# Performance work log

Hardware: AMD Instinct MI355X
Metric: run time of the kernel (lower is better)

## Reference

```python
import jax, jax.numpy as jnp
import numpy as np

B, S, D = 4, 2048, 1024
H = 8  # hardcoded in AttentionLayer
HD = D // H
FF = 4096
EPS = 1e-5


def _layernorm(x):
    # LayerNorm(hidden_dim, elementwise_affine=False), eps=1e-5
    mu = jnp.mean(x, axis=-1, keepdims=True)
    var = jnp.var(x, axis=-1, keepdims=True)
    return (x - mu) / jnp.sqrt(var + EPS)


def setup_inputs() -> dict:
    key = jax.random.key(0)
    ks = jax.random.split(key, 5)
    scale = 0.02
    return {
        "x": jax.random.normal(ks[0], (B, S, D), dtype=jnp.float32),
        "qkv_proj": jax.random.normal(ks[1], (D, 3 * D), dtype=jnp.float32) * scale,
        "o_proj": jax.random.normal(ks[2], (D, D), dtype=jnp.float32) * scale,
        "ff1": jax.random.normal(ks[3], (D, FF), dtype=jnp.float32) * scale,
        "ff2": jax.random.normal(ks[4], (FF, D), dtype=jnp.float32) * scale,
    }


def reference(x, qkv_proj, o_proj, ff1, ff2):
    b, s, d = x.shape
    # --- attention ---
    qkv = jnp.matmul(x, qkv_proj)                       # [b,s,3d]
    qkv = qkv.reshape(b, s, H, 3 * HD).transpose(0, 2, 1, 3)  # [b,h,s,3hd]
    q, k, v = jnp.split(qkv, 3, axis=-1)                # each [b,h,s,hd]
    logits = jnp.einsum('bhqd,bhkd->bhqk', q, k) / jnp.sqrt(jnp.float32(HD))
    attn = jax.nn.softmax(logits, axis=-1)
    vals = jnp.einsum('bhqk,bhkd->bhqd', attn, v)       # [b,h,s,hd]
    vals = vals.transpose(0, 2, 1, 3).reshape(b, s, d)
    attn_out = jnp.matmul(vals, o_proj)
    # --- residual + norm + FFN + residual + norm ---
    x = _layernorm(x + attn_out)
    ff_out = jnp.matmul(jax.nn.relu(jnp.matmul(x, ff1)), ff2)
    x = _layernorm(x + ff_out)
    return x
```

## Files before the change

kernel.cpp:

```cpp
#include <hip/hip_runtime.h>
#include <hip/hip_bf16.h>


typedef float floatx4 __attribute__((ext_vector_type(4)));
typedef float floatx16 __attribute__((ext_vector_type(16)));
typedef short bf16x8 __attribute__((ext_vector_type(8)));

#define DEVI __device__ __forceinline__

typedef const __attribute__((address_space(1))) unsigned int* gas1_t;
typedef __attribute__((address_space(3))) unsigned int* las3_t;

DEVI void gll16(const void* g, void* l) {
  __builtin_amdgcn_global_load_lds((gas1_t)g, (las3_t)l, 16, 0, 0);
}

DEVI short bfbits(float f) {
  __hip_bfloat16 h = __float2bfloat16(f);
  return *reinterpret_cast<short*>(&h);
}

DEVI unsigned int packbf(float lo, float hi) {
  return __builtin_amdgcn_perm(__float_as_uint(hi) + 0x8000u,
                               __float_as_uint(lo) + 0x8000u,
                               0x07060302u);
}

template<int EPI, int SPLITK>
__global__ __launch_bounds__(256, 4) void gemm_bt(
    const __hip_bfloat16* __restrict__ A,
    const __hip_bfloat16* __restrict__ BT,
    float* __restrict__ Cf, float* __restrict__ Cf2,
    __hip_bfloat16* __restrict__ Cb,
    int M, int N, int K)
{
  __shared__ __hip_bfloat16 As[128 * 64];
  __shared__ __hip_bfloat16 Bs[128 * 64];
  const int tid = threadIdx.x;
  const int wave = tid >> 6, lane = tid & 63;
  const int lane15 = lane & 15, quad = lane >> 4;
  const int row0 = blockIdx.x * 128, col0 = blockIdx.y * 128;
  const int wr = (wave >> 1) * 64, wc = (wave & 1) * 64;
  const int Kh = K / SPLITK;
  const size_t kofs = (SPLITK > 1) ? (size_t)blockIdx.z * Kh : 0;

  floatx4 acc[4][4] = {};

  const int srow = tid >> 3;
  const int sblk = (tid & 7) ^ (srow & 7);
  const __hip_bfloat16* Ag = A + (size_t)(row0 + srow) * K + kofs + sblk * 8;
  const __hip_bfloat16* Bg = BT + (size_t)(col0 + srow) * K + kofs + sblk * 8;
  char* Asl = (char*)As + tid * 16;
  char* Bsl = (char*)Bs + tid * 16;
  const size_t rstep = (size_t)32 * K;

  const int x7 = lane15 & 7;
  for (int k0 = 0; k0 < Kh; k0 += 64) {
    __syncthreads();
#pragma unroll
    for (int p = 0; p < 4; p++) {
      gll16(Ag + k0 + p * rstep, Asl + p * 4096);
      gll16(Bg + k0 + p * rstep, Bsl + p * 4096);
    }
    __syncthreads();
#pragma unroll
    for (int kc = 0; kc < 2; kc++) {
      bf16x8 af[4], bb[4];
#pragma unroll
      for (int t = 0; t < 4; t++) {
        const int r = wr + t * 16 + lane15;
        af[t] = *(const bf16x8*)((const char*)As + r * 128 + (((kc * 4 + quad) ^ x7) << 4));
      }
#pragma unroll
      for (int t = 0; t < 4; t++) {
        const int r = wc + t * 16 + lane15;
        bb[t] = *(const bf16x8*)((const char*)Bs + r * 128 + (((kc * 4 + quad) ^ x7) << 4));
      }
#pragma unroll
      for (int i = 0; i < 4; i++)
#pragma unroll
        for (int j = 0; j < 4; j++)
          acc[i][j] = __builtin_amdgcn_mfma_f32_16x16x32_bf16(af[i], bb[j], acc[i][j], 0, 0, 0);
    }
  }

  float* Cp = (SPLITK > 1 && blockIdx.z) ? Cf2 : Cf;
#pragma unroll
  for (int i = 0; i < 4; i++) {
    const int mb = row0 + wr + i * 16 + quad * 4;
#pragma unroll
    for (int j = 0; j < 4; j++) {
      const int n = col0 + wc + j * 16 + lane15;
#pragma unroll
      for (int r = 0; r < 4; r++) {
        const size_t idx = (size_t)(mb + r) * N + n;
        const float v = acc[i][j][r];
        if (EPI == 0) {
          Cb[idx] = __float2bfloat16(v);
        } else if (EPI == 2) {
          Cb[idx] = __float2bfloat16(v > 0.f ? v : 0.f);
        } else {
          Cp[idx] = v;
        }
      }
    }
  }
}

__global__ __launch_bounds__(256, 2) void attn_kernel(
    const __hip_bfloat16* __restrict__ qkv,
    const __hip_bfloat16* __restrict__ Vt,
    __hip_bfloat16* __restrict__ vals)
{
  __shared__ __hip_bfloat16 Ak[128 * 128];
  __shared__ __hip_bfloat16 Bq[128 * 128];

  const int tid = threadIdx.x;
  const int wave = tid >> 6, lane = tid & 63;
  const int l31 = lane & 31, l5 = lane >> 5;
  const int bh = blockIdx.x, qt = blockIdx.y;
  const int b = bh >> 3, h = bh & 7;
  const size_t tokbase = (size_t)b * 2048;
  const float scale = 0.08838834764831845f;

  const int sw8 = ((tid & 15) ^ (tid >> 4)) * 8;
  const int srow = tid >> 4;
  const __hip_bfloat16* qg  = qkv + (tokbase + qt * 128) * 3072 + h * 384 + sw8;
  const __hip_bfloat16* kg0 = qkv + tokbase * 3072 + h * 384 + 128 + sw8;
  const __hip_bfloat16* vg0 = Vt + (size_t)bh * 128 * 2048 + sw8;

#pragma unroll
  for (int rd = 0; rd < 8; rd++)
    gll16(qg + (size_t)(rd * 16 + srow) * 3072, (char*)Bq + rd * 4096 + tid * 16);
  __syncthreads();

  const int rx = l31 & 15;
  bf16x8 qf[8];
  {
    const char* qb = (const char*)Bq + (wave * 32 + l31) * 256;
#pragma unroll
    for (int ks = 0; ks < 8; ks++)
      qf[ks] = *(const bf16x8*)(qb + (((ks * 2 + l5) ^ rx) << 4));
  }
#pragma unroll
  for (int rd = 0; rd < 8; rd++)
    gll16(kg0 + (size_t)(rd * 16 + srow) * 3072, (char*)Ak + rd * 4096 + tid * 16);
  __syncthreads();

  floatx16 oacc[4] = {};
  float lsum = 0.f;

  for (int kt = 0; kt < 16; kt++) {
    if (kt) __syncthreads();

#pragma unroll
    for (int rd = 0; rd < 8; rd++)
      gll16(vg0 + (size_t)kt * 128 + (size_t)(rd * 16 + srow) * 2048,
            (char*)Bq + rd * 4096 + tid * 16);

    floatx16 sacc[4] = {};
#pragma unroll
    for (int ks = 0; ks < 8; ks++) {
      const int off = ((ks * 2 + l5) ^ rx) << 4;
      const char* kb = (const char*)Ak + l31 * 256 + off;
#pragma unroll
      for (int nt = 0; nt < 4; nt++) {
        const bf16x8 ak = *(const bf16x8*)(kb + nt * 8192);
        sacc[nt] = __builtin_amdgcn_mfma_f32_32x32x16_bf16(ak, qf[ks], sacc[nt], 0, 0, 0);
      }
    }

    unsigned int pk0[16], pk1[16];
#pragma unroll
    for (int idx = 0; idx < 16; idx++) {
      const int nt = idx >> 2, g4 = (idx & 3) * 4;
      const float p0 = __expf(sacc[nt][g4 + 0] * scale);
      const float p1 = __expf(sacc[nt][g4 + 1] * scale);
      const float p2 = __expf(sacc[nt][g4 + 2] * scale);
      const float p3 = __expf(sacc[nt][g4 + 3] * scale);
      lsum += (p0 + p1) + (p2 + p3);
      pk0[idx] = packbf(p0, p1);
      pk1[idx] = packbf(p2, p3);
    }
    bf16x8 pf[8];
#pragma unroll
    for (int ks = 0; ks < 8; ks++) {
      const unsigned int own0 = l5 ? pk0[ks * 2 + 1] : pk0[ks * 2];
      const unsigned int own1 = l5 ? pk1[ks * 2 + 1] : pk1[ks * 2];
      const unsigned int snd0 = l5 ? pk0[ks * 2] : pk0[ks * 2 + 1];
      const unsigned int snd1 = l5 ? pk1[ks * 2] : pk1[ks * 2 + 1];
      const unsigned int rc0 = (unsigned int)__shfl_xor((int)snd0, 32);
      const unsigned int rc1 = (unsigned int)__shfl_xor((int)snd1, 32);
      union { int4 i; bf16x8 v; } u;
      u.i.x = l5 ? (int)rc0 : (int)own0;
      u.i.y = l5 ? (int)rc1 : (int)own1;
      u.i.z = l5 ? (int)own0 : (int)rc0;
      u.i.w = l5 ? (int)own1 : (int)rc1;
      pf[ks] = u.v;
    }

    __syncthreads();
    if (kt < 15) {
#pragma unroll
      for (int rd = 0; rd < 8; rd++)
        gll16(kg0 + (size_t)((kt + 1) * 128 + rd * 16 + srow) * 3072,
              (char*)Ak + rd * 4096 + tid * 16);
    }

#pragma unroll
    for (int ks = 0; ks < 8; ks++) {
      const int off = ((ks * 2 + l5) ^ rx) << 4;
      const char* vb = (const char*)Bq + l31 * 256 + off;
#pragma unroll
      for (int nt = 0; nt < 4; nt++) {
        const bf16x8 av = *(const bf16x8*)(vb + nt * 8192);
        oacc[nt] = __builtin_amdgcn_mfma_f32_32x32x16_bf16(av, pf[ks], oacc[nt], 0, 0, 0);
      }
    }
  }

  lsum += __shfl_xor(lsum, 32);
  const float linv = 1.f / lsum;

  const size_t row = tokbase + (size_t)qt * 128 + wave * 32 + l31;
  __hip_bfloat16* vrow = vals + row * 1024 + h * 128 + 4 * l5;
#pragma unroll
  for (int nt = 0; nt < 4; nt++)
#pragma unroll
    for (int g = 0; g < 4; g++) {
      uint2 pk;
      pk.x = packbf(oacc[nt][g * 4 + 0] * linv, oacc[nt][g * 4 + 1] * linv);
      pk.y = packbf(oacc[nt][g * 4 + 2] * linv, oacc[nt][g * 4 + 3] * linv);
      *(uint2*)(vrow + nt * 32 + g * 8) = pk;
    }
}

__global__ __launch_bounds__(256) void prep_k(
    const float* __restrict__ x, __hip_bfloat16* __restrict__ xb,
    const float* __restrict__ qkvw, __hip_bfloat16* __restrict__ qkvT,
    const float* __restrict__ ow, __hip_bfloat16* __restrict__ oT,
    const float* __restrict__ f1, __hip_bfloat16* __restrict__ f1T,
    const float* __restrict__ f2, __hip_bfloat16* __restrict__ f2T)
{
  const int bid = blockIdx.x;
  if (bid < 8192) {
    const size_t i = (size_t)bid * 256 + threadIdx.x;
    const float4 v = ((const float4*)x)[i];
    short4 sv;
    sv.x = bfbits(v.x); sv.y = bfbits(v.y); sv.z = bfbits(v.z); sv.w = bfbits(v.w);
    ((short4*)xb)[i] = sv;
    return;
  }
  int t = bid - 8192;
  const float* W; __hip_bfloat16* WT; int K, N, nbx;
  if (t < 3072) { W = qkvw; WT = qkvT; K = 1024; N = 3072; nbx = 96; }
  else if (t < 3072 + 1024) { t -= 3072; W = ow; WT = oT; K = 1024; N = 1024; nbx = 32; }
  else if (t < 3072 + 1024 + 4096) { t -= 3072 + 1024; W = f1; WT = f1T; K = 1024; N = 4096; nbx = 128; }
  else { t -= 3072 + 1024 + 4096; W = f2; WT = f2T; K = 4096; N = 1024; nbx = 32; }
  __shared__ float tl[32][33];
  const int tx = threadIdx.x & 31, ty = threadIdx.x >> 5;
  const int n0 = (t % nbx) * 32, k0 = (t / nbx) * 32;
#pragma unroll
  for (int i = 0; i < 4; i++)
    tl[ty + i * 8][tx] = W[(size_t)(k0 + ty + i * 8) * N + n0 + tx];
  __syncthreads();
#pragma unroll
  for (int i = 0; i < 4; i++)
    WT[(size_t)(n0 + ty + i * 8) * K + k0 + tx] = __float2bfloat16(tl[tx][ty + i * 8]);
}

__global__ __launch_bounds__(256) void vtrans_k(const __hip_bfloat16* __restrict__ qkv,
                                                __hip_bfloat16* __restrict__ Vt) {
  __shared__ __hip_bfloat16 t[32][33];
  const int tx = threadIdx.x & 31, ty = threadIdx.x >> 5;
  const int s0 = blockIdx.x * 32, d0 = blockIdx.y * 32, bh = blockIdx.z;
  const int b = bh >> 3, h = bh & 7;
#pragma unroll
  for (int i = 0; i < 4; i++)
    t[ty + i * 8][tx] = qkv[((size_t)b * 2048 + s0 + ty + i * 8) * 3072 + h * 384 + 256 + d0 + tx];
  __syncthreads();
#pragma unroll
  for (int i = 0; i < 4; i++)
    Vt[((size_t)bh * 128 + d0 + ty + i * 8) * 2048 + s0 + tx] = t[tx][ty + i * 8];
}

template<bool RES_BF16, bool FINAL>
__global__ __launch_bounds__(256) void ln_red_k(
    const float* __restrict__ p0, const float* __restrict__ p1,
    const float* __restrict__ resf, const __hip_bfloat16* __restrict__ resb,
    __hip_bfloat16* __restrict__ ob, float* __restrict__ of) {
  const int row = blockIdx.x, tid = threadIdx.x;
  const size_t base = (size_t)row * 1024;
  const float4 a = ((const float4*)(p0 + base))[tid];
  const float4 bb = ((const float4*)(p1 + base))[tid];
  float4 v;
  if (RES_BF16) {
    const short4 rb = ((const short4*)(resb + base))[tid];
    v.x = a.x + bb.x + __bfloat162float(*(const __hip_bfloat16*)&rb.x);
    v.y = a.y + bb.y + __bfloat162float(*(const __hip_bfloat16*)&rb.y);
    v.z = a.z + bb.z + __bfloat162float(*(const __hip_bfloat16*)&rb.z);
    v.w = a.w + bb.w + __bfloat162float(*(const __hip_bfloat16*)&rb.w);
  } else {
    const float4 rf = ((const float4*)(resf + base))[tid];
    v.x = a.x + bb.x + rf.x; v.y = a.y + bb.y + rf.y;
    v.z = a.z + bb.z + rf.z; v.w = a.w + bb.w + rf.w;
  }
  float s = v.x + v.y + v.z + v.w;
  float q = v.x * v.x + v.y * v.y + v.z * v.z + v.w * v.w;
#pragma unroll
  for (int off = 32; off; off >>= 1) { s += __shfl_xor(s, off); q += __shfl_xor(q, off); }
  __shared__ float ss[4], sq[4];
  const int wave = tid >> 6;
  if ((tid & 63) == 0) { ss[wave] = s; sq[wave] = q; }
  __syncthreads();
  s = ss[0] + ss[1] + ss[2] + ss[3];
  q = sq[0] + sq[1] + sq[2] + sq[3];
  const float mean = s * (1.f / 1024.f);
  const float var = q * (1.f / 1024.f) - mean * mean;
  const float rstd = rsqrtf(var + 1e-5f);
  float4 o;
  o.x = (v.x - mean) * rstd; o.y = (v.y - mean) * rstd;
  o.z = (v.z - mean) * rstd; o.w = (v.w - mean) * rstd;
  if (FINAL) {
    ((float4*)(of + base))[tid] = o;
  } else {
    short4 sv;
    sv.x = bfbits(o.x); sv.y = bfbits(o.y); sv.z = bfbits(o.z); sv.w = bfbits(o.w);
    ((short4*)(ob + base))[tid] = sv;
  }
}

extern "C" void kernel_launch(void* const* d_in, const int* in_sizes, int n_in,
                              void* d_out, int out_size, void* d_ws, size_t ws_size,
                              hipStream_t stream) {
  const float* x    = (const float*)d_in[0];
  const float* qkvw = (const float*)d_in[1];
  const float* ow   = (const float*)d_in[2];
  const float* f1   = (const float*)d_in[3];
  const float* f2   = (const float*)d_in[4];
  float* out = (float*)d_out;

  char* ws = (char*)d_ws;
  const size_t MB = 1024 * 1024;
  __hip_bfloat16* xb   = (__hip_bfloat16*)(ws);
  __hip_bfloat16* vals = xb;
  float*          P1f  = (float*)(ws);
  __hip_bfloat16* qkvT = (__hip_bfloat16*)(ws + 16 * MB);
  __hip_bfloat16* oT   = (__hip_bfloat16*)(ws + 22 * MB);
  __hip_bfloat16* f1T  = (__hip_bfloat16*)(ws + 24 * MB);
  __hip_bfloat16* f2T  = (__hip_bfloat16*)(ws + 32 * MB);
  __hip_bfloat16* qkvb = (__hip_bfloat16*)(ws + 40 * MB);
  __hip_bfloat16* Vt   = (__hip_bfloat16*)(ws + 88 * MB);
  float*          P0o  = (float*)(ws + 40 * MB);
  float*          P1o  = (float*)(ws + 72 * MB);
  __hip_bfloat16* hmid = (__hip_bfloat16*)(ws + 40 * MB);
  float*          P0f  = (float*)(ws + 104 * MB);
  __hip_bfloat16* x1b  = (__hip_bfloat16*)(ws + 136 * MB);
  (void)in_sizes; (void)n_in; (void)out_size; (void)ws_size;

  prep_k<<<20480, 256, 0, stream>>>(x, xb, qkvw, qkvT, ow, oT, f1, f1T, f2, f2T);
  gemm_bt<0, 1><<<dim3(64, 24, 1), 256, 0, stream>>>(xb, qkvT, nullptr, nullptr,
                                                     qkvb, 8192, 3072, 1024);
  vtrans_k<<<dim3(64, 4, 32), 256, 0, stream>>>(qkvb, Vt);
  attn_kernel<<<dim3(32, 16), 256, 0, stream>>>(qkvb, Vt, vals);
  gemm_bt<4, 2><<<dim3(64, 8, 2), 256, 0, stream>>>(vals, oT, P0o, P1o,
                                                    nullptr, 8192, 1024, 1024);
  ln_red_k<false, false><<<8192, 256, 0, stream>>>(P0o, P1o, x, nullptr, x1b, nullptr);
  gemm_bt<2, 1><<<dim3(64, 32, 1), 256, 0, stream>>>(x1b, f1T, nullptr, nullptr,
                                                     hmid, 8192, 4096, 1024);
  gemm_bt<4, 2><<<dim3(64, 8, 2), 256, 0, stream>>>(hmid, f2T, P0f, P1f,
                                                    nullptr, 8192, 1024, 4096);
  ln_red_k<true, true><<<8192, 256, 0, stream>>>(P0f, P1f, nullptr, x1b, nullptr, out);
}
```

Measured before the change: 456.2 us.

## Store split-K partials in bf16, prescale Q for exp2, and permute K rows to skip shuffles

Split-K GEMM partial outputs and the residual input to the first layernorm become bf16 instead of fp32, which halves traffic for those intermediates. The Q columns are pre-multiplied by scale*log2(e) in the QKV GEMM epilogue, so attention can call exp2f directly. K rows are loaded in a permuted order so each lane already holds the P values it needs for the PV MFMA, removing the cross-half-wave shuffles. The residual for the first layernorm now comes from the bf16 copy of x rather than fp32 x, which lowers accuracy.

```diff
diff --git a/kernel.cpp b/kernel.cpp
--- a/kernel.cpp
+++ b/kernel.cpp
@@ -30,8 +30,7 @@
 __global__ __launch_bounds__(256, 4) void gemm_bt(
     const __hip_bfloat16* __restrict__ A,
     const __hip_bfloat16* __restrict__ BT,
-    float* __restrict__ Cf, float* __restrict__ Cf2,
-    __hip_bfloat16* __restrict__ Cb,
+    __hip_bfloat16* __restrict__ Cb, __hip_bfloat16* __restrict__ Cb2,
     int M, int N, int K)
 {
   __shared__ __hip_bfloat16 As[128 * 64];
@@ -84,23 +83,24 @@
     }
   }
 
-  float* Cp = (SPLITK > 1 && blockIdx.z) ? Cf2 : Cf;
+  __hip_bfloat16* Cp = (SPLITK > 1 && blockIdx.z) ? Cb2 : Cb;
 #pragma unroll
   for (int i = 0; i < 4; i++) {
     const int mb = row0 + wr + i * 16 + quad * 4;
 #pragma unroll
     for (int j = 0; j < 4; j++) {
       const int n = col0 + wc + j * 16 + lane15;
+      const float fac = (EPI == 0 && (((n >> 7) % 3) == 0)) ? 0.12751729f : 1.f;
 #pragma unroll
       for (int r = 0; r < 4; r++) {
         const size_t idx = (size_t)(mb + r) * N + n;
         const float v = acc[i][j][r];
         if (EPI == 0) {
-          Cb[idx] = __float2bfloat16(v);
+          Cb[idx] = __float2bfloat16(v * fac);
         } else if (EPI == 2) {
           Cb[idx] = __float2bfloat16(v > 0.f ? v : 0.f);
         } else {
-          Cp[idx] = v;
+          Cp[idx] = __float2bfloat16(v);
         }
       }
     }
@@ -121,10 +121,10 @@
   const int bh = blockIdx.x, qt = blockIdx.y;
   const int b = bh >> 3, h = bh & 7;
   const size_t tokbase = (size_t)b * 2048;
-  const float scale = 0.08838834764831845f;
 
   const int sw8 = ((tid & 15) ^ (tid >> 4)) * 8;
   const int srow = tid >> 4;
+  const int srowp = (srow & 3) | ((srow << 1) & 8) | ((srow >> 1) & 4);
   const __hip_bfloat16* qg  = qkv + (tokbase + qt * 128) * 3072 + h * 384 + sw8;
   const __hip_bfloat16* kg0 = qkv + tokbase * 3072 + h * 384 + 128 + sw8;
   const __hip_bfloat16* vg0 = Vt + (size_t)bh * 128 * 2048 + sw8;
@@ -144,7 +144,7 @@
   }
 #pragma unroll
   for (int rd = 0; rd < 8; rd++)
-    gll16(kg0 + (size_t)(rd * 16 + srow) * 3072, (char*)Ak + rd * 4096 + tid * 16);
+    gll16(kg0 + (size_t)(rd * 16 + srowp) * 3072, (char*)Ak + rd * 4096 + tid * 16);
   __syncthreads();
 
   floatx16 oacc[4] = {};
@@ -170,40 +170,30 @@
       }
     }
 
-    unsigned int pk0[16], pk1[16];
-#pragma unroll
-    for (int idx = 0; idx < 16; idx++) {
-      const int nt = idx >> 2, g4 = (idx & 3) * 4;
-      const float p0 = __expf(sacc[nt][g4 + 0] * scale);
-      const float p1 = __expf(sacc[nt][g4 + 1] * scale);
-      const float p2 = __expf(sacc[nt][g4 + 2] * scale);
-      const float p3 = __expf(sacc[nt][g4 + 3] * scale);
-      lsum += (p0 + p1) + (p2 + p3);
-      pk0[idx] = packbf(p0, p1);
-      pk1[idx] = packbf(p2, p3);
-    }
     bf16x8 pf[8];
 #pragma unroll
-    for (int ks = 0; ks < 8; ks++) {
-      const unsigned int own0 = l5 ? pk0[ks * 2 + 1] : pk0[ks * 2];
-      const unsigned int own1 = l5 ? pk1[ks * 2 + 1] : pk1[ks * 2];
-      const unsigned int snd0 = l5 ? pk0[ks * 2] : pk0[ks * 2 + 1];
-      const unsigned int snd1 = l5 ? pk1[ks * 2] : pk1[ks * 2 + 1];
-      const unsigned int rc0 = (unsigned int)__shfl_xor((int)snd0, 32);
-      const unsigned int rc1 = (unsigned int)__shfl_xor((int)snd1, 32);
-      union { int4 i; bf16x8 v; } u;
-      u.i.x = l5 ? (int)rc0 : (int)own0;
-      u.i.y = l5 ? (int)rc1 : (int)own1;
-      u.i.z = l5 ? (int)own0 : (int)rc0;
-      u.i.w = l5 ? (int)own1 : (int)rc1;
-      pf[ks] = u.v;
+    for (int c = 0; c < 8; c++) {
+      const int nt = c >> 1, bi = (c & 1) * 8;
+      const float p0 = exp2f(sacc[nt][bi + 0]);
+      const float p1 = exp2f(sacc[nt][bi + 1]);
+      const float p2 = exp2f(sacc[nt][bi + 2]);
+      const float p3 = exp2f(sacc[nt][bi + 3]);
+      const float p4 = exp2f(sacc[nt][bi + 4]);
+      const float p5 = exp2f(sacc[nt][bi + 5]);
+      const float p6 = exp2f(sacc[nt][bi + 6]);
+      const float p7 = exp2f(sacc[nt][bi + 7]);
+      lsum += ((p0 + p1) + (p2 + p3)) + ((p4 + p5) + (p6 + p7));
+      union { uint4 u; bf16x8 v; } w;
+      w.u.x = packbf(p0, p1); w.u.y = packbf(p2, p3);
+      w.u.z = packbf(p4, p5); w.u.w = packbf(p6, p7);
+      pf[c] = w.v;
     }
 
     __syncthreads();
     if (kt < 15) {
 #pragma unroll
       for (int rd = 0; rd < 8; rd++)
-        gll16(kg0 + (size_t)((kt + 1) * 128 + rd * 16 + srow) * 3072,
+        gll16(kg0 + (size_t)((kt + 1) * 128 + rd * 16 + srowp) * 3072,
               (char*)Ak + rd * 4096 + tid * 16);
     }
 
@@ -284,27 +274,23 @@
     Vt[((size_t)bh * 128 + d0 + ty + i * 8) * 2048 + s0 + tx] = t[tx][ty + i * 8];
 }
 
-template<bool RES_BF16, bool FINAL>
+template<bool FINAL>
 __global__ __launch_bounds__(256) void ln_red_k(
-    const float* __restrict__ p0, const float* __restrict__ p1,
-    const float* __restrict__ resf, const __hip_bfloat16* __restrict__ resb,
+    const __hip_bfloat16* __restrict__ p0, const __hip_bfloat16* __restrict__ p1,
+    const __hip_bfloat16* __restrict__ res,
     __hip_bfloat16* __restrict__ ob, float* __restrict__ of) {
   const int row = blockIdx.x, tid = threadIdx.x;
   const size_t base = (size_t)row * 1024;
-  const float4 a = ((const float4*)(p0 + base))[tid];
-  const float4 bb = ((const float4*)(p1 + base))[tid];
+  const short4 a4 = ((const short4*)(p0 + base))[tid];
+  const short4 b4 = ((const short4*)(p1 + base))[tid];
+  const short4 r4 = ((const short4*)(res + base))[tid];
+#define BF(x) __bfloat162float(*(const __hip_bfloat16*)&(x))
   float4 v;
-  if (RES_BF16) {
-    const short4 rb = ((const short4*)(resb + base))[tid];
-    v.x = a.x + bb.x + __bfloat162float(*(const __hip_bfloat16*)&rb.x);
-    v.y = a.y + bb.y + __bfloat162float(*(const __hip_bfloat16*)&rb.y);
-    v.z = a.z + bb.z + __bfloat162float(*(const __hip_bfloat16*)&rb.z);
-    v.w = a.w + bb.w + __bfloat162float(*(const __hip_bfloat16*)&rb.w);
-  } else {
-    const float4 rf = ((const float4*)(resf + base))[tid];
-    v.x = a.x + bb.x + rf.x; v.y = a.y + bb.y + rf.y;
-    v.z = a.z + bb.z + rf.z; v.w = a.w + bb.w + rf.w;
-  }
+  v.x = BF(a4.x) + BF(b4.x) + BF(r4.x);
+  v.y = BF(a4.y) + BF(b4.y) + BF(r4.y);
+  v.z = BF(a4.z) + BF(b4.z) + BF(r4.z);
+  v.w = BF(a4.w) + BF(b4.w) + BF(r4.w);
+#undef BF
   float s = v.x + v.y + v.z + v.w;
   float q = v.x * v.x + v.y * v.y + v.z * v.z + v.w * v.w;
 #pragma unroll
@@ -343,32 +329,32 @@
   char* ws = (char*)d_ws;
   const size_t MB = 1024 * 1024;
   __hip_bfloat16* xb   = (__hip_bfloat16*)(ws);
-  __hip_bfloat16* vals = xb;
-  float*          P1f  = (float*)(ws);
-  __hip_bfloat16* qkvT = (__hip_bfloat16*)(ws + 16 * MB);
-  __hip_bfloat16* oT   = (__hip_bfloat16*)(ws + 22 * MB);
-  __hip_bfloat16* f1T  = (__hip_bfloat16*)(ws + 24 * MB);
-  __hip_bfloat16* f2T  = (__hip_bfloat16*)(ws + 32 * MB);
-  __hip_bfloat16* qkvb = (__hip_bfloat16*)(ws + 40 * MB);
-  __hip_bfloat16* Vt   = (__hip_bfloat16*)(ws + 88 * MB);
-  float*          P0o  = (float*)(ws + 40 * MB);
-  float*          P1o  = (float*)(ws + 72 * MB);
-  __hip_bfloat16* hmid = (__hip_bfloat16*)(ws + 40 * MB);
-  float*          P0f  = (float*)(ws + 104 * MB);
-  __hip_bfloat16* x1b  = (__hip_bfloat16*)(ws + 136 * MB);
+  __hip_bfloat16* vals = (__hip_bfloat16*)(ws + 16 * MB);
+  __hip_bfloat16* P1f  = (__hip_bfloat16*)(ws + 16 * MB);
+  __hip_bfloat16* qkvT = (__hip_bfloat16*)(ws + 32 * MB);
+  __hip_bfloat16* oT   = (__hip_bfloat16*)(ws + 38 * MB);
+  __hip_bfloat16* f1T  = (__hip_bfloat16*)(ws + 40 * MB);
+  __hip_bfloat16* f2T  = (__hip_bfloat16*)(ws + 48 * MB);
+  __hip_bfloat16* qkvb = (__hip_bfloat16*)(ws + 56 * MB);
+  __hip_bfloat16* P0o  = (__hip_bfloat16*)(ws + 56 * MB);
+  __hip_bfloat16* P1o  = (__hip_bfloat16*)(ws + 72 * MB);
+  __hip_bfloat16* hmid = (__hip_bfloat16*)(ws + 56 * MB);
+  __hip_bfloat16* Vt   = (__hip_bfloat16*)(ws + 104 * MB);
+  __hip_bfloat16* x1b  = (__hip_bfloat16*)(ws + 120 * MB);
+  __hip_bfloat16* P0f  = (__hip_bfloat16*)(ws + 136 * MB);
   (void)in_sizes; (void)n_in; (void)out_size; (void)ws_size;
 
   prep_k<<<20480, 256, 0, stream>>>(x, xb, qkvw, qkvT, ow, oT, f1, f1T, f2, f2T);
-  gemm_bt<0, 1><<<dim3(64, 24, 1), 256, 0, stream>>>(xb, qkvT, nullptr, nullptr,
-                                                     qkvb, 8192, 3072, 1024);
+  gemm_bt<0, 1><<<dim3(64, 24, 1), 256, 0, stream>>>(xb, qkvT, qkvb, nullptr,
+                                                     8192, 3072, 1024);
   vtrans_k<<<dim3(64, 4, 32), 256, 0, stream>>>(qkvb, Vt);
   attn_kernel<<<dim3(32, 16), 256, 0, stream>>>(qkvb, Vt, vals);
   gemm_bt<4, 2><<<dim3(64, 8, 2), 256, 0, stream>>>(vals, oT, P0o, P1o,
-                                                    nullptr, 8192, 1024, 1024);
-  ln_red_k<false, false><<<8192, 256, 0, stream>>>(P0o, P1o, x, nullptr, x1b, nullptr);
-  gemm_bt<2, 1><<<dim3(64, 32, 1), 256, 0, stream>>>(x1b, f1T, nullptr, nullptr,
-                                                     hmid, 8192, 4096, 1024);
+                                                    8192, 1024, 1024);
+  ln_red_k<false><<<8192, 256, 0, stream>>>(P0o, P1o, xb, x1b, nullptr);
+  gemm_bt<2, 1><<<dim3(64, 32, 1), 256, 0, stream>>>(x1b, f1T, hmid, nullptr,
+                                                     8192, 4096, 1024);
   gemm_bt<4, 2><<<dim3(64, 8, 2), 256, 0, stream>>>(hmid, f2T, P0f, P1f,
-                                                    nullptr, 8192, 1024, 4096);
-  ln_red_k<true, true><<<8192, 256, 0, stream>>>(P0f, P1f, nullptr, x1b, nullptr, out);
-}
+                                                    8192, 1024, 4096);
+  ln_red_k<true><<<8192, 256, 0, stream>>>(P0f, P1f, x1b, nullptr, out);
+}
```

Measured after the change: 441.8 us. 1.03x faster.
